# Kernel tuning notes

Measured on AMD Instinct MI355X. Metric: run time of the kernel, lower is better.

Reference implementation:

```python
import jax, jax.numpy as jnp
import numpy as np

H, W = 256, 256
N = H * W
C0, C1, C2 = 16, 32, 64  # base, base*2, base*4


def _grid_edges(h, w):
    """8-neighborhood grid edges (directed, both directions) + self loops."""
    idx = np.arange(h * w).reshape(h, w)
    srcs, dsts = [], []
    for dy in (-1, 0, 1):
        for dx in (-1, 0, 1):
            if dy == 0 and dx == 0:
                continue
            s = idx[max(0, -dy):h - max(0, dy), max(0, -dx):w - max(0, dx)]
            d = idx[max(0, dy):h - max(0, -dy), max(0, dx):w - max(0, -dx)]
            srcs.append(s.ravel()); dsts.append(d.ravel())
    srcs.append(np.arange(h * w)); dsts.append(np.arange(h * w))  # GATConv add_self_loops
    return np.concatenate(srcs).astype(np.int32), np.concatenate(dsts).astype(np.int32)


def _conv2d(x, w, b, pad):
    y = jax.lax.conv_general_dilated(x, w, (1, 1), [(pad, pad), (pad, pad)],
                                     dimension_numbers=('NCHW', 'OIHW', 'NCHW'))
    return y + b[None, :, None, None]


def _bn(x, g, b, eps=1e-5):
    # training-mode BatchNorm2d: biased batch statistics over (N,H,W)
    mu = x.mean((0, 2, 3), keepdims=True)
    var = ((x - mu) ** 2).mean((0, 2, 3), keepdims=True)
    return g[None, :, None, None] * (x - mu) * jax.lax.rsqrt(var + eps) + b[None, :, None, None]


def _gat(xg, w, a_s, a_d, b, src, dst):
    # PyG GATConv, heads=1: gather -> leaky_relu attention -> softmax over dst -> scatter-add
    def one(xn):
        h = xn @ w.T                                   # [N, C_out]
        e = jax.nn.leaky_relu((h @ a_s)[src] + (h @ a_d)[dst], 0.2)  # [E]
        m = jax.ops.segment_max(e, dst, num_segments=N)
        p = jnp.exp(e - m[dst])
        denom = jax.ops.segment_sum(p, dst, num_segments=N)
        agg = jax.ops.segment_sum(h[src] * p[:, None], dst, num_segments=N)
        return agg / (denom[:, None] + 1e-16) + b
    return jax.vmap(one)(xg)


def _gcb(x, pos_w, pos_b, gw, gas, gad, gb, src, dst):
    B, C = x.shape[0], x.shape[1]
    px = jnp.linspace(-1.0, 1.0, W)
    py = jnp.linspace(-1.0, 1.0, H)
    gx, gy = jnp.meshgrid(px, py, indexing='xy')       # each (H, W)
    pos = jnp.stack([gy, gx], -1)                      # (H, W, 2)
    pe = pos @ pos_w.T + pos_b                         # (H, W, C)
    x = x + pe.transpose(2, 0, 1)[None]
    xg = x.transpose(0, 2, 3, 1).reshape(B, N, C)      # batch of disjoint graphs -> vmap
    out = _gat(xg, gw, gas, gad, gb, src, dst)
    return out.reshape(B, H, W, -1).transpose(0, 3, 1, 2)


def _forward(x, conv1_w, conv1_b, bn1_g, bn1_b,
             pos1_w, pos1_b, gat1_w, gat1_as, gat1_ad, gat1_b, bn2_g, bn2_b,
             pos2_w, pos2_b, gat2_w, gat2_as, gat2_ad, gat2_b, bn3_g, bn3_b,
             mlp1_w, mlp1_b, mlp2_w, mlp2_b, filt, filt_bias,
             enh1_w, enh1_b, enh2_w, enh2_b, bn4_g, bn4_b, src, dst):
    f = _bn(jax.nn.relu(_conv2d(x, conv1_w, conv1_b, 2)), bn1_g, bn1_b)
    f = _bn(jax.nn.relu(_gcb(f, pos1_w, pos1_b, gat1_w, gat1_as, gat1_ad, gat1_b, src, dst)), bn2_g, bn2_b)
    f = _bn(jax.nn.relu(_gcb(f, pos2_w, pos2_b, gat2_w, gat2_as, gat2_ad, gat2_b, src, dst)), bn3_g, bn3_b)
    pooled = f.mean((2, 3))                            # AdaptiveAvgPool2d(1)
    h = jax.nn.relu(pooled @ mlp1_w.T + mlp1_b)
    cw = jax.nn.softmax(h @ mlp2_w.T + mlp2_b, axis=1)[:, :, None, None]
    wf = f * cw
    ff = wf * filt + filt_bias
    enh = _conv2d(jax.nn.relu(_conv2d(ff, enh1_w, enh1_b, 1)), enh2_w, enh2_b, 1) + ff
    return _bn(jax.nn.relu(enh), bn4_g, bn4_b)


def setup_inputs() -> dict:
    key = jax.random.key(0)
    ks = iter(jax.random.split(key, 40))
    def rn(shape, s=0.1):
        return jax.random.normal(next(ks), shape, dtype=jnp.float32) * s
    src, dst = _grid_edges(H, W)
    return {
        'x': jax.random.normal(next(ks), (2, 1, H, W), dtype=jnp.float32),
        'conv1_w': rn((C0, 1, 5, 5)), 'conv1_b': rn((C0,)),
        'bn1_g': jnp.ones((C0,)), 'bn1_b': jnp.zeros((C0,)),
        'pos1_w': rn((C0, 2)), 'pos1_b': rn((C0,)),
        'gat1_w': rn((C1, C0)), 'gat1_as': rn((C1,)), 'gat1_ad': rn((C1,)), 'gat1_b': rn((C1,)),
        'bn2_g': jnp.ones((C1,)), 'bn2_b': jnp.zeros((C1,)),
        'pos2_w': rn((C1, 2)), 'pos2_b': rn((C1,)),
        'gat2_w': rn((C2, C1)), 'gat2_as': rn((C2,)), 'gat2_ad': rn((C2,)), 'gat2_b': rn((C2,)),
        'bn3_g': jnp.ones((C2,)), 'bn3_b': jnp.zeros((C2,)),
        'mlp1_w': rn((C2 // 4, C2)), 'mlp1_b': rn((C2 // 4,)),
        'mlp2_w': rn((C2, C2 // 4)), 'mlp2_b': rn((C2,)),
        'filt': jnp.ones((1, C2, H, W)), 'filt_bias': jnp.zeros((1, C2, 1, 1)),
        'enh1_w': rn((C2 // 2, C2, 3, 3)), 'enh1_b': rn((C2 // 2,)),
        'enh2_w': rn((C2, C2 // 2, 3, 3)), 'enh2_b': rn((C2,)),
        'bn4_g': jnp.ones((C2,)), 'bn4_b': jnp.zeros((C2,)),
        'src': jnp.asarray(src), 'dst': jnp.asarray(dst),
    }


def reference(x, conv1_w, conv1_b, bn1_g, bn1_b,
              pos1_w, pos1_b, gat1_w, gat1_as, gat1_ad, gat1_b, bn2_g, bn2_b,
              pos2_w, pos2_b, gat2_w, gat2_as, gat2_ad, gat2_b, bn3_g, bn3_b,
              mlp1_w, mlp1_b, mlp2_w, mlp2_b, filt, filt_bias,
              enh1_w, enh1_b, enh2_w, enh2_b, bn4_g, bn4_b, src, dst):
    return _forward(x, conv1_w, conv1_b, bn1_g, bn1_b,
                    pos1_w, pos1_b, gat1_w, gat1_as, gat1_ad, gat1_b, bn2_g, bn2_b,
                    pos2_w, pos2_b, gat2_w, gat2_as, gat2_ad, gat2_b, bn3_g, bn3_b,
                    mlp1_w, mlp1_b, mlp2_w, mlp2_b, filt, filt_bias,
                    enh1_w, enh1_b, enh2_w, enh2_b, bn4_g, bn4_b, src, dst)
```

## Files before the change

kernel.cpp:

```cpp
#include <hip/hip_runtime.h>
#include <math.h>

#define HH 256
#define WW 256
#define NPIX 65536
#define BATCH 2

#define OFF_W0   0u
#define OFF_W1   8388608u
#define OFF_W2   16777216u
#define OFF_W3   20971520u
#define OFF_S    25165824u
#define OFF_D    25296896u
#define OFF_STAT 25427968u
#define OFF_ST1  (OFF_STAT + 0u)
#define OFF_ST2  (OFF_STAT + 64u)
#define OFF_ST3  (OFF_STAT + 192u)
#define OFF_ST4  (OFF_STAT + 448u)
#define OFF_CW   (OFF_STAT + 576u)
#define STAT_ZERO_N 704
#define OFF_WB1  (OFF_STAT + 704u)
#define OFF_WB2  (OFF_WB1 + 18432u)

typedef __attribute__((ext_vector_type(8))) short bf8v;
typedef __attribute__((ext_vector_type(4))) float f4v;
typedef __attribute__((ext_vector_type(4))) unsigned short us4;

#define GLL16(g, l) __builtin_amdgcn_global_load_lds(                               \
    (const __attribute__((address_space(1))) unsigned int*)(g),                    \
    (__attribute__((address_space(3))) unsigned int*)(l), 16, 0, 0)

__device__ __forceinline__ unsigned short f2bf(float f) {
    unsigned u = __float_as_uint(f);
    return (unsigned short)((u + 0x7FFFu + ((u >> 16) & 1u)) >> 16);
}
__device__ __forceinline__ float bf2f(unsigned short u) {
    return __uint_as_float(((unsigned)u) << 16);
}

__device__ __forceinline__ void bn_coef(const float* __restrict__ raw,
                                        const float* __restrict__ g,
                                        const float* __restrict__ b,
                                        int C, int c, float& A, float& Bv) {
    const float inv = 1.f / (float)(BATCH * NPIX);
    float mu  = raw[c] * inv;
    float var = raw[C + c] * inv - mu * mu;
    float rinv = rsqrtf(var + 1e-5f);
    A  = g[c] * rinv;
    Bv = b[c] - A * mu;
}

__device__ __forceinline__ void wave_red2(float& s, float& q) {
#pragma unroll
    for (int off = 32; off; off >>= 1) {
        s += __shfl_xor(s, off);
        q += __shfl_xor(q, off);
    }
}

__device__ __forceinline__ void row_swz512(int bid, int& y, int& b) {
    int orig = (bid & 7) * 64 + (bid >> 3);
    y = orig & 255;
    b = orig >> 8;
}

__global__ void prep(float* __restrict__ st,
                     const float* __restrict__ w1, unsigned short* __restrict__ wb1,
                     const float* __restrict__ w2, unsigned short* __restrict__ wb2) {
    int bid = blockIdx.x, tid = threadIdx.x;
    if (bid < 3) {
        int i = bid * 256 + tid;
        if (i < STAT_ZERO_N) st[i] = 0.f;
    } else if (bid < 75) {
        int i = (bid - 3) * 256 + tid;
        int co = i / (64 * 9);
        int rem = i - co * 64 * 9;
        int ci = rem / 9;
        int pos = rem - ci * 9;
        wb1[(pos * 32 + co) * 64 + ci] = f2bf(w1[i]);
    } else {
        int i = (bid - 75) * 256 + tid;
        int co = i / (32 * 9);
        int rem = i - co * 32 * 9;
        int ci = rem / 9;
        int pos = rem - ci * 9;
        wb2[(pos * 64 + co) * 32 + ci] = f2bf(w2[i]);
    }
}

__global__ __launch_bounds__(256) void conv5x5_all(const float* __restrict__ x,
                                                   const float* __restrict__ w,
                                                   const float* __restrict__ bias,
                                                   unsigned short* __restrict__ out,
                                                   float* __restrict__ st) {
    int y = blockIdx.x, b = blockIdx.y;
    int xx = threadIdx.x;
    __shared__ float lds[5 * 260];
    __shared__ float red[2][16][4];
    for (int i = threadIdx.x; i < 5 * 260; i += 256) {
        int r = i / 260, pos = i - r * 260;
        int yy = y + r - 2, xc = pos - 2;
        float v = 0.f;
        if ((unsigned)yy < 256u && (unsigned)xc < 256u) v = x[(b << 16) + (yy << 8) + xc];
        lds[i] = v;
    }
    __syncthreads();
    float v[25];
#pragma unroll
    for (int r = 0; r < 5; r++)
#pragma unroll
        for (int c = 0; c < 5; c++) v[r * 5 + c] = lds[r * 260 + xx + c];
    int lane = threadIdx.x & 63, wv = threadIdx.x >> 6;
#pragma unroll
    for (int co = 0; co < 16; co++) {
        float acc = bias[co];
#pragma unroll
        for (int k = 0; k < 25; k++) acc = fmaf(v[k], w[co * 25 + k], acc);
        acc = fmaxf(acc, 0.f);
        out[((size_t)(b * 16 + co) << 16) + (y << 8) + xx] = f2bf(acc);
        float s = acc, q = acc * acc;
        wave_red2(s, q);
        if (lane == 0) { red[0][co][wv] = s; red[1][co][wv] = q; }
    }
    __syncthreads();
    if (threadIdx.x < 16) {
        int co = threadIdx.x;
        float s = red[0][co][0] + red[0][co][1] + red[0][co][2] + red[0][co][3];
        float q = red[1][co][0] + red[1][co][1] + red[1][co][2] + red[1][co][3];
        atomicAdd(&st[co], s);
        atomicAdd(&st[16 + co], q);
    }
}

template <int CI, int CO>
__global__ void gat_pre(const unsigned short* __restrict__ f, const float* __restrict__ raw,
                        const float* __restrict__ bng, const float* __restrict__ bnb,
                        const float* __restrict__ posw, const float* __restrict__ posb,
                        const float* __restrict__ gw, const float* __restrict__ gas,
                        const float* __restrict__ gad,
                        unsigned short* __restrict__ hout, float* __restrict__ sout,
                        float* __restrict__ dout) {
    int tid = blockIdx.x * 256 + threadIdx.x;
    int n = tid & (NPIX - 1);
    int b = tid >> 16;
    int y = n >> 8, x = n & 255;
    float py = y * (2.f / 255.f) - 1.f;
    float px = x * (2.f / 255.f) - 1.f;
    float v[CI];
#pragma unroll
    for (int ci = 0; ci < CI; ci++) {
        float A, Bv;
        bn_coef(raw, bng, bnb, CI, ci, A, Bv);
        float t = fmaf(bf2f(f[(size_t)(b * CI + ci) * NPIX + n]), A, Bv);
        v[ci] = t + posw[2 * ci] * py + posw[2 * ci + 1] * px + posb[ci];
    }
    float s = 0.f, d = 0.f;
    for (int co = 0; co < CO; co++) {
        float acc = 0.f;
#pragma unroll
        for (int ci = 0; ci < CI; ci++) acc = fmaf(v[ci], gw[co * CI + ci], acc);
        hout[(size_t)(b * CO + co) * NPIX + n] = f2bf(acc);
        s = fmaf(acc, gas[co], s);
        d = fmaf(acc, gad[co], d);
    }
    sout[tid] = s;
    dout[tid] = d;
}

template <int CO, bool POOL>
__global__ __launch_bounds__(256) void gat_stencil_mfma(const unsigned short* __restrict__ hb,
                                                        const float* __restrict__ sbuf,
                                                        const float* __restrict__ dbuf,
                                                        const float* __restrict__ gb,
                                                        unsigned short* __restrict__ out,
                                                        float* __restrict__ st) {
    constexpr int NT = CO / 16;
    int y, b;
    row_swz512(blockIdx.x, y, b);
    int tid = threadIdx.x, lane = tid & 63, wid = tid >> 6;
    int m = lane & 15, grp = lane >> 4;
    int xw = wid * 64;
    {
        int x = xw + lane;
        float di = dbuf[(b << 16) + (y << 8) + x];
        float p[9], mx = -1e30f;
#pragma unroll
        for (int k = 0; k < 9; k++) {
            int dy = k / 3 - 1, dx = k % 3 - 1;
            int yy = y + dy, xx = x + dx;
            bool ok = ((unsigned)yy < 256u) && ((unsigned)xx < 256u);
            float e = -1e30f;
            if (ok) {
                float t = sbuf[(b << 16) + (yy << 8) + xx] + di;
                e = t > 0.f ? t : 0.2f * t;
            }
            p[k] = e;
            mx = fmaxf(mx, e);
        }
        float den = 0.f;
#pragma unroll
        for (int k = 0; k < 9; k++) { p[k] = __expf(p[k] - mx); den += p[k]; }
        float rden = 1.f / (den + 1e-16f);
        unsigned short pb[9];
#pragma unroll
        for (int k = 0; k < 9; k++) pb[k] = f2bf(p[k] * rden);
        unsigned pk0 = (unsigned)pb[0] | ((unsigned)pb[1] << 16);
        unsigned pk1 = (unsigned)pb[2] | ((unsigned)pb[3] << 16);
        unsigned pk2 = (unsigned)pb[4] | ((unsigned)pb[5] << 16);
        unsigned pk3 = (unsigned)pb[6] | ((unsigned)pb[7] << 16);
        unsigned pk4 = (unsigned)pb[8];
        float sAcc[NT], qAcc[NT], bb[NT];
#pragma unroll
        for (int ct = 0; ct < NT; ct++) { sAcc[ct] = 0.f; qAcc[ct] = 0.f; bb[ct] = gb[ct * 16 + m]; }

#pragma unroll 1
        for (int t = 0; t < 4; t++) {
            int xb = xw + t * 16;
            int src = t * 16 + m;
            unsigned rk0 = __shfl(pk0, src);
            unsigned rk1 = __shfl(pk1, src);
            unsigned rk2 = __shfl(pk2, src);
            unsigned rk3 = __shfl(pk3, src);
            unsigned rk4 = __shfl(pk4, src);
            unsigned short rb[9];
            rb[0] = (unsigned short)rk0; rb[1] = (unsigned short)(rk0 >> 16);
            rb[2] = (unsigned short)rk1; rb[3] = (unsigned short)(rk1 >> 16);
            rb[4] = (unsigned short)rk2; rb[5] = (unsigned short)(rk2 >> 16);
            rb[6] = (unsigned short)rk3; rb[7] = (unsigned short)(rk3 >> 16);
            rb[8] = (unsigned short)rk4;
            union { bf8v v; unsigned short h[8]; } af[3];
#pragma unroll
            for (int dyi = 0; dyi < 3; dyi++)
#pragma unroll
                for (int j = 0; j < 8; j++) {
                    int k = grp * 8 + j;
                    int d = k - 8 - m;
                    af[dyi].h[j] = (d >= -1 && d <= 1) ? rb[dyi * 3 + d + 1] : (unsigned short)0;
                }
            f4v acc[NT];
            f4v z4 = {0.f, 0.f, 0.f, 0.f};
#pragma unroll
            for (int ct = 0; ct < NT; ct++) acc[ct] = z4;
            int px0 = xb - 8 + grp * 8;
            px0 = px0 < 0 ? 0 : (px0 > 248 ? 248 : px0);
#pragma unroll
            for (int dyi = 0; dyi < 3; dyi++) {
                int yy = y + dyi - 1;
                if ((unsigned)yy >= 256u) continue;
#pragma unroll
                for (int ct = 0; ct < NT; ct++) {
                    bf8v bv = *(const bf8v*)(hb + (((size_t)(b * CO + ct * 16 + m)) << 16) + (yy << 8) + px0);
                    acc[ct] = __builtin_amdgcn_mfma_f32_16x16x32_bf16(af[dyi].v, bv, acc[ct], 0, 0, 0);
                }
            }
            int pxr = xb + grp * 4;
#pragma unroll
            for (int ct = 0; ct < NT; ct++) {
                f4v a = acc[ct];
                float o0 = fmaxf(a[0] + bb[ct], 0.f);
                float o1 = fmaxf(a[1] + bb[ct], 0.f);
                float o2 = fmaxf(a[2] + bb[ct], 0.f);
                float o3 = fmaxf(a[3] + bb[ct], 0.f);
                us4 pkst = {f2bf(o0), f2bf(o1), f2bf(o2), f2bf(o3)};
                *(us4*)(out + (((size_t)(b * CO + ct * 16 + m)) << 16) + (y << 8) + pxr) = pkst;
                sAcc[ct] += o0 + o1 + o2 + o3;
                qAcc[ct] += o0 * o0 + o1 * o1 + o2 * o2 + o3 * o3;
            }
        }
#pragma unroll
        for (int ct = 0; ct < NT; ct++) {
            sAcc[ct] += __shfl_xor(sAcc[ct], 16); sAcc[ct] += __shfl_xor(sAcc[ct], 32);
            qAcc[ct] += __shfl_xor(qAcc[ct], 16); qAcc[ct] += __shfl_xor(qAcc[ct], 32);
        }
        __shared__ float red[2][NT][16][4];
        if (grp == 0) {
#pragma unroll
            for (int ct = 0; ct < NT; ct++) {
                red[0][ct][m][wid] = sAcc[ct];
                red[1][ct][m][wid] = qAcc[ct];
            }
        }
        __syncthreads();
        if (tid < CO) {
            int ct = tid >> 4, mm = tid & 15;
            float s = red[0][ct][mm][0] + red[0][ct][mm][1] + red[0][ct][mm][2] + red[0][ct][mm][3];
            float qq = red[1][ct][mm][0] + red[1][ct][mm][1] + red[1][ct][mm][2] + red[1][ct][mm][3];
            atomicAdd(&st[tid], s);
            atomicAdd(&st[CO + tid], qq);
            if (POOL) atomicAdd(&st[2 * CO + b * CO + tid], s);
        }
    }
}

__global__ void mlp_cw(const float* __restrict__ raw3, const float* __restrict__ g3,
                       const float* __restrict__ b3, const float* __restrict__ w1,
                       const float* __restrict__ bb1, const float* __restrict__ w2,
                       const float* __restrict__ bb2, float* __restrict__ cw) {
    __shared__ float pooled[2][64];
    __shared__ float hsh[2][16];
    int tid = threadIdx.x;
    {
        int b = tid >> 6, c = tid & 63;
        float A, Bv;
        bn_coef(raw3, g3, b3, 64, c, A, Bv);
        float sm = raw3[128 + (b << 6) + c];
        pooled[b][c] = fmaf(sm * (1.f / 65536.f), A, Bv);
    }
    __syncthreads();
    if (tid < 32) {
        int b = tid >> 4, j = tid & 15;
        float acc = bb1[j];
        for (int c2 = 0; c2 < 64; c2++) acc = fmaf(pooled[b][c2], w1[(j << 6) + c2], acc);
        hsh[b][j] = fmaxf(acc, 0.f);
    }
    __syncthreads();
    int b = tid >> 6, c = tid & 63;
    float logit = bb2[c];
    for (int j = 0; j < 16; j++) logit = fmaf(hsh[b][j], w2[(c << 4) + j], logit);
    float mm = logit;
#pragma unroll
    for (int off = 32; off; off >>= 1) mm = fmaxf(mm, __shfl_xor(mm, off));
    float e = __expf(logit - mm);
    float ss = e;
#pragma unroll
    for (int off = 32; off; off >>= 1) ss += __shfl_xor(ss, off);
    cw[(b << 6) + c] = e / ss;
}

__global__ __launch_bounds__(256) void ff_t(const unsigned short* __restrict__ g64,
                                            const float* __restrict__ raw3,
                                            const float* __restrict__ g3,
                                            const float* __restrict__ b3,
                                            const float* __restrict__ cw,
                                            const float* __restrict__ filt,
                                            const float* __restrict__ fbias,
                                            float* __restrict__ ffout,
                                            unsigned* __restrict__ at1) {
    int pxb = blockIdx.x * 64;
    int b = pxb >> 16;
    int nb = pxb & 65535;
    __shared__ unsigned t[64 * 33];
    int tid = threadIdx.x;
#pragma unroll
    for (int k = 0; k < 2; k++) {
        int u = tid + k * 256;
        int q = u & 15;
        int cp = u >> 4;
        int ch0 = cp * 2, ch1 = ch0 + 1;
        float A0, B0, A1, B1;
        bn_coef(raw3, g3, b3, 64, ch0, A0, B0);
        bn_coef(raw3, g3, b3, 64, ch1, A1, B1);
        float s0 = cw[(b << 6) + ch0], s1 = cw[(b << 6) + ch1];
        float fb0 = fbias[ch0], fb1 = fbias[ch1];
        int n = nb + q * 4;
        us4 r0 = *(const us4*)(g64 + ((size_t)(b * 64 + ch0) << 16) + n);
        us4 r1 = *(const us4*)(g64 + ((size_t)(b * 64 + ch1) << 16) + n);
        float4 l0 = *(const float4*)(filt + ((size_t)ch0 << 16) + n);
        float4 l1 = *(const float4*)(filt + ((size_t)ch1 << 16) + n);
        float4 o0, o1;
        o0.x = fmaf(fmaf(bf2f(r0[0]), A0, B0) * s0, l0.x, fb0);
        o0.y = fmaf(fmaf(bf2f(r0[1]), A0, B0) * s0, l0.y, fb0);
        o0.z = fmaf(fmaf(bf2f(r0[2]), A0, B0) * s0, l0.z, fb0);
        o0.w = fmaf(fmaf(bf2f(r0[3]), A0, B0) * s0, l0.w, fb0);
        o1.x = fmaf(fmaf(bf2f(r1[0]), A1, B1) * s1, l1.x, fb1);
        o1.y = fmaf(fmaf(bf2f(r1[1]), A1, B1) * s1, l1.y, fb1);
        o1.z = fmaf(fmaf(bf2f(r1[2]), A1, B1) * s1, l1.z, fb1);
        o1.w = fmaf(fmaf(bf2f(r1[3]), A1, B1) * s1, l1.w, fb1);
        *(float4*)(ffout + ((size_t)(b * 64 + ch0) << 16) + n) = o0;
        *(float4*)(ffout + ((size_t)(b * 64 + ch1) << 16) + n) = o1;
        float e0[4] = {o0.x, o0.y, o0.z, o0.w};
        float e1[4] = {o1.x, o1.y, o1.z, o1.w};
#pragma unroll
        for (int i = 0; i < 4; i++)
            t[(q * 4 + i) * 33 + cp] = (unsigned)f2bf(e0[i]) | ((unsigned)f2bf(e1[i]) << 16);
    }
    __syncthreads();
#pragma unroll
    for (int j = 0; j < 8; j++) {
        int lin = j * 256 + tid;
        int pl = lin >> 5, cp = lin & 31;
        unsigned v = t[pl * 33 + cp];
        int P = pxb + pl;
        size_t byte = ((size_t)P << 7) + ((cp >= 16) ? 64 : 0)
                    + (((cp & 15) * 4) ^ (((P >> 1) & 3) << 4));
        *(unsigned*)((char*)at1 + byte) = v;
    }
}

__global__ __launch_bounds__(256) void enh1_mfma(const unsigned short* __restrict__ at1,
                                                 const unsigned short* __restrict__ wb,
                                                 const float* __restrict__ bias,
                                                 unsigned short* __restrict__ at2) {
    int y, b;
    row_swz512(blockIdx.x, y, b);
    int tid = threadIdx.x;
    int lane = tid & 63, wid = tid >> 6;
    __shared__ __align__(16) unsigned short lds_u16[3 * 258 * 32];
    char* ldsb = (char*)lds_u16;
    {
        bf8v z = {0, 0, 0, 0, 0, 0, 0, 0};
        for (int i = tid; i < 3 * 258 * 32 / 8; i += 256) ((bf8v*)lds_u16)[i] = z;
    }
    f4v acc[4][2];
    {
        f4v z4 = {0.f, 0.f, 0.f, 0.f};
#pragma unroll
        for (int m = 0; m < 4; m++) { acc[m][0] = z4; acc[m][1] = z4; }
    }
#pragma unroll 1
    for (int kh = 0; kh < 2; kh++) {
        __syncthreads();
        for (int c = wid; c < 48; c += 4) {
            int r = c >> 4, k = c & 15;
            int yy = y + r - 1;
            if ((unsigned)yy < 256u) {
                const char* src = (const char*)at1
                    + (((size_t)((b << 16) + (yy << 8)) + (k * 16 + (lane >> 2))) << 7)
                    + kh * 64 + (lane & 3) * 16;
                char* dst = ldsb + (r * 258 + 1) * 64 + k * 1024;
                GLL16(src, dst);
            }
        }
        __syncthreads();
        bf8v bw0[9], bw1[9];
#pragma unroll
        for (int pos = 0; pos < 9; pos++) {
            bw0[pos] = *(const bf8v*)(wb + (pos * 32 + (lane & 15)) * 64 + kh * 32 + (lane >> 4) * 8);
            bw1[pos] = *(const bf8v*)(wb + (pos * 32 + 16 + (lane & 15)) * 64 + kh * 32 + (lane >> 4) * 8);
        }
#pragma unroll
        for (int mt = 0; mt < 4; mt++) {
            int xb = (wid * 4 + mt) * 16 + (lane & 15);
#pragma unroll
            for (int ky = 0; ky < 3; ky++) {
#pragma unroll
                for (int kx = 0; kx < 3; kx++) {
                    int x = xb + kx - 1;
                    int s = x + 1;
                    int off = (ky * 258 + s) * 64 + (((lane >> 4) * 16) ^ (((x >> 1) & 3) << 4));
                    bf8v a = *(const bf8v*)(ldsb + off);
                    acc[mt][0] = __builtin_amdgcn_mfma_f32_16x16x32_bf16(a, bw0[ky * 3 + kx], acc[mt][0], 0, 0, 0);
                    acc[mt][1] = __builtin_amdgcn_mfma_f32_16x16x32_bf16(a, bw1[ky * 3 + kx], acc[mt][1], 0, 0, 0);
                }
            }
        }
    }
    float bb[2] = {bias[lane & 15], bias[16 + (lane & 15)]};
#pragma unroll
    for (int mt = 0; mt < 4; mt++) {
#pragma unroll
        for (int nt = 0; nt < 2; nt++) {
            f4v v = acc[mt][nt];
            int co = nt * 16 + (lane & 15);
#pragma unroll
            for (int r = 0; r < 4; r++) {
                int x = (wid * 4 + mt) * 16 + (lane >> 4) * 4 + r;
                float val = fmaxf(v[r] + bb[nt], 0.f);
                size_t byte = (((size_t)((b << 16) + (y << 8) + x)) << 6)
                            + ((co * 2) ^ (((x >> 1) & 3) << 4));
                *(unsigned short*)((char*)at2 + byte) = f2bf(val);
            }
        }
    }
}

__global__ __launch_bounds__(256) void enh2_mfma(const unsigned short* __restrict__ at2,
                                                 const unsigned short* __restrict__ wb,
                                                 const float* __restrict__ bias,
                                                 const float* __restrict__ ff,
                                                 float* __restrict__ out,
                                                 float* __restrict__ st) {
    int y, b;
    row_swz512(blockIdx.x, y, b);
    int tid = threadIdx.x;
    int lane = tid & 63, wid = tid >> 6;
    __shared__ __align__(16) unsigned short lds_u16[3 * 258 * 32];
    char* ldsb = (char*)lds_u16;
    {
        bf8v z = {0, 0, 0, 0, 0, 0, 0, 0};
        for (int i = tid; i < 3 * 258 * 32 / 8; i += 256) ((bf8v*)lds_u16)[i] = z;
    }
    __syncthreads();
    for (int c = wid; c < 48; c += 4) {
        int r = c >> 4, k = c & 15;
        int yy = y + r - 1;
        if ((unsigned)yy < 256u) {
            const char* src = (const char*)at2
                + (((size_t)((b << 16) + (yy << 8))) << 6) + k * 1024 + lane * 16;
            char* dst = ldsb + (r * 258 + 1) * 64 + k * 1024;
            GLL16(src, dst);
        }
    }
    __syncthreads();
    f4v acc[4][4];
    {
        f4v z4 = {0.f, 0.f, 0.f, 0.f};
#pragma unroll
        for (int m = 0; m < 4; m++)
#pragma unroll
            for (int n = 0; n < 4; n++) acc[m][n] = z4;
    }
#pragma unroll
    for (int np = 0; np < 2; np++) {
        bf8v bw0[9], bw1[9];
#pragma unroll
        for (int pos = 0; pos < 9; pos++) {
            bw0[pos] = *(const bf8v*)(wb + (pos * 64 + np * 32 + (lane & 15)) * 32 + (lane >> 4) * 8);
            bw1[pos] = *(const bf8v*)(wb + (pos * 64 + np * 32 + 16 + (lane & 15)) * 32 + (lane >> 4) * 8);
        }
#pragma unroll
        for (int mt = 0; mt < 4; mt++) {
            int xb = (wid * 4 + mt) * 16 + (lane & 15);
#pragma unroll
            for (int ky = 0; ky < 3; ky++) {
#pragma unroll
                for (int kx = 0; kx < 3; kx++) {
                    int x = xb + kx - 1;
                    int s = x + 1;
                    int off = (ky * 258 + s) * 64 + (((lane >> 4) * 16) ^ (((x >> 1) & 3) << 4));
                    bf8v a = *(const bf8v*)(ldsb + off);
                    acc[mt][2 * np]     = __builtin_amdgcn_mfma_f32_16x16x32_bf16(a, bw0[ky * 3 + kx], acc[mt][2 * np], 0, 0, 0);
                    acc[mt][2 * np + 1] = __builtin_amdgcn_mfma_f32_16x16x32_bf16(a, bw1[ky * 3 + kx], acc[mt][2 * np + 1], 0, 0, 0);
                }
            }
        }
    }
    __syncthreads();
    float* red = (float*)lds_u16;
#pragma unroll
    for (int nt = 0; nt < 4; nt++) {
        int co = nt * 16 + (lane & 15);
        float bb = bias[co];
        float s = 0.f, q = 0.f;
#pragma unroll
        for (int mt = 0; mt < 4; mt++) {
            int xb4 = (wid * 4 + mt) * 16 + (lane >> 4) * 4;
            size_t idx = ((size_t)(b * 64 + co) << 16) + (y << 8) + xb4;
            float4 res = *(const float4*)(ff + idx);
            f4v a = acc[mt][nt];
            float4 o;
            o.x = fmaxf(a[0] + bb + res.x, 0.f);
            o.y = fmaxf(a[1] + bb + res.y, 0.f);
            o.z = fmaxf(a[2] + bb + res.z, 0.f);
            o.w = fmaxf(a[3] + bb + res.w, 0.f);
            *(float4*)(out + idx) = o;
            s += o.x + o.y + o.z + o.w;
            q += o.x * o.x + o.y * o.y + o.z * o.z + o.w * o.w;
        }
        s += __shfl_xor(s, 16); s += __shfl_xor(s, 32);
        q += __shfl_xor(q, 16); q += __shfl_xor(q, 32);
        if (lane < 16) {
            red[(co * 4 + wid) * 2 + 0] = s;
            red[(co * 4 + wid) * 2 + 1] = q;
        }
    }
    __syncthreads();
    if (tid < 64) {
        float s = 0.f, q = 0.f;
#pragma unroll
        for (int w = 0; w < 4; w++) {
            s += red[(tid * 4 + w) * 2 + 0];
            q += red[(tid * 4 + w) * 2 + 1];
        }
        atomicAdd(&st[tid], s);
        atomicAdd(&st[64 + tid], q);
    }
}

__global__ void bn_apply4(float4* __restrict__ io, const float* __restrict__ raw,
                          const float* __restrict__ g, const float* __restrict__ b) {
    int t = blockIdx.x * 256 + threadIdx.x;
    int c = (t >> 14) & 63;
    float A, Bv;
    bn_coef(raw, g, b, 64, c, A, Bv);
    float4 v = io[t];
    v.x = fmaf(v.x, A, Bv);
    v.y = fmaf(v.y, A, Bv);
    v.z = fmaf(v.z, A, Bv);
    v.w = fmaf(v.w, A, Bv);
    io[t] = v;
}

extern "C" void kernel_launch(void* const* d_in, const int* in_sizes, int n_in,
                              void* d_out, int out_size, void* d_ws, size_t ws_size,
                              hipStream_t stream) {
    const float* x       = (const float*)d_in[0];
    const float* conv1_w = (const float*)d_in[1];
    const float* conv1_b = (const float*)d_in[2];
    const float* bn1_g   = (const float*)d_in[3];
    const float* bn1_b   = (const float*)d_in[4];
    const float* pos1_w  = (const float*)d_in[5];
    const float* pos1_b  = (const float*)d_in[6];
    const float* gat1_w  = (const float*)d_in[7];
    const float* gat1_as = (const float*)d_in[8];
    const float* gat1_ad = (const float*)d_in[9];
    const float* gat1_b  = (const float*)d_in[10];
    const float* bn2_g   = (const float*)d_in[11];
    const float* bn2_b   = (const float*)d_in[12];
    const float* pos2_w  = (const float*)d_in[13];
    const float* pos2_b  = (const float*)d_in[14];
    const float* gat2_w  = (const float*)d_in[15];
    const float* gat2_as = (const float*)d_in[16];
    const float* gat2_ad = (const float*)d_in[17];
    const float* gat2_b  = (const float*)d_in[18];
    const float* bn3_g   = (const float*)d_in[19];
    const float* bn3_b   = (const float*)d_in[20];
    const float* mlp1_w  = (const float*)d_in[21];
    const float* mlp1_b  = (const float*)d_in[22];
    const float* mlp2_w  = (const float*)d_in[23];
    const float* mlp2_b  = (const float*)d_in[24];
    const float* filt    = (const float*)d_in[25];
    const float* fbias   = (const float*)d_in[26];
    const float* enh1_w  = (const float*)d_in[27];
    const float* enh1_b  = (const float*)d_in[28];
    const float* enh2_w  = (const float*)d_in[29];
    const float* enh2_b  = (const float*)d_in[30];
    const float* bn4_g   = (const float*)d_in[31];
    const float* bn4_b   = (const float*)d_in[32];

    float* ws = (float*)d_ws;
    unsigned short* P0 = (unsigned short*)(ws + OFF_W0);
    unsigned short* HB = (unsigned short*)(ws + OFF_W1);
    float* FF = ws + OFF_W1;
    unsigned* AT1 = (unsigned*)(ws + OFF_W2);
    unsigned short* AT2 = (unsigned short*)(ws + OFF_W3);
    float* SB = ws + OFF_S;
    float* DB = ws + OFF_D;
    float* ST1 = ws + OFF_ST1;
    float* ST2 = ws + OFF_ST2;
    float* ST3 = ws + OFF_ST3;
    float* ST4 = ws + OFF_ST4;
    float* CW  = ws + OFF_CW;
    unsigned short* WB1 = (unsigned short*)(ws + OFF_WB1);
    unsigned short* WB2 = (unsigned short*)(ws + OFF_WB2);
    float* out = (float*)d_out;

    prep<<<147, 256, 0, stream>>>(ws + OFF_STAT, enh1_w, WB1, enh2_w, WB2);

    conv5x5_all<<<dim3(256, 2), 256, 0, stream>>>(x, conv1_w, conv1_b, P0, ST1);

    gat_pre<16, 32><<<512, 256, 0, stream>>>(P0, ST1, bn1_g, bn1_b, pos1_w, pos1_b,
                                             gat1_w, gat1_as, gat1_ad, HB, SB, DB);

    gat_stencil_mfma<32, false><<<512, 256, 0, stream>>>(HB, SB, DB, gat1_b, P0, ST2);

    gat_pre<32, 64><<<512, 256, 0, stream>>>(P0, ST2, bn2_g, bn2_b, pos2_w, pos2_b,
                                             gat2_w, gat2_as, gat2_ad, HB, SB, DB);

    gat_stencil_mfma<64, true><<<512, 256, 0, stream>>>(HB, SB, DB, gat2_b, P0, ST3);

    mlp_cw<<<1, 128, 0, stream>>>(ST3, bn3_g, bn3_b, mlp1_w, mlp1_b, mlp2_w, mlp2_b, CW);

    ff_t<<<2048, 256, 0, stream>>>(P0, ST3, bn3_g, bn3_b, CW, filt, fbias, FF, AT1);

    enh1_mfma<<<512, 256, 0, stream>>>((const unsigned short*)AT1, WB1, enh1_b, AT2);

    enh2_mfma<<<512, 256, 0, stream>>>(AT2, WB2, enh2_b, FF, out, ST4);

    bn_apply4<<<32768 / 4, 256, 0, stream>>>((float4*)out, ST4, bn4_g, bn4_b);
}
```

Before: 197.0 us.

## Split GAT stencil blocks by channel half and store FF residual as bf16

```diff
diff --git a/kernel.cpp b/kernel.cpp
--- a/kernel.cpp
+++ b/kernel.cpp
@@ -174,121 +174,129 @@
                                                         const float* __restrict__ gb,
                                                         unsigned short* __restrict__ out,
                                                         float* __restrict__ st) {
-    constexpr int NT = CO / 16;
-    int y, b;
-    row_swz512(blockIdx.x, y, b);
+    constexpr int NT2 = CO / 32;
+    constexpr int CH = CO / 2;
+    int bid = blockIdx.x;
+    int orig = (bid & 7) * 128 + (bid >> 3);
+    int coh = orig & 1;
+    int rowu = orig >> 1;
+    int y = rowu & 255;
+    int b = rowu >> 8;
     int tid = threadIdx.x, lane = tid & 63, wid = tid >> 6;
     int m = lane & 15, grp = lane >> 4;
     int xw = wid * 64;
-    {
-        int x = xw + lane;
-        float di = dbuf[(b << 16) + (y << 8) + x];
-        float p[9], mx = -1e30f;
-#pragma unroll
-        for (int k = 0; k < 9; k++) {
-            int dy = k / 3 - 1, dx = k % 3 - 1;
-            int yy = y + dy, xx = x + dx;
-            bool ok = ((unsigned)yy < 256u) && ((unsigned)xx < 256u);
-            float e = -1e30f;
-            if (ok) {
-                float t = sbuf[(b << 16) + (yy << 8) + xx] + di;
-                e = t > 0.f ? t : 0.2f * t;
+    int x = xw + lane;
+    float di = dbuf[(b << 16) + (y << 8) + x];
+    float p[9], mx = -1e30f;
+#pragma unroll
+    for (int k = 0; k < 9; k++) {
+        int dy = k / 3 - 1, dx = k % 3 - 1;
+        int yy = y + dy, xxn = x + dx;
+        bool ok = ((unsigned)yy < 256u) && ((unsigned)xxn < 256u);
+        float e = -1e30f;
+        if (ok) {
+            float t = sbuf[(b << 16) + (yy << 8) + xxn] + di;
+            e = t > 0.f ? t : 0.2f * t;
+        }
+        p[k] = e;
+        mx = fmaxf(mx, e);
+    }
+    float den = 0.f;
+#pragma unroll
+    for (int k = 0; k < 9; k++) { p[k] = __expf(p[k] - mx); den += p[k]; }
+    float rden = 1.f / (den + 1e-16f);
+    unsigned short pb[9];
+#pragma unroll
+    for (int k = 0; k < 9; k++) pb[k] = f2bf(p[k] * rden);
+    unsigned pk0 = (unsigned)pb[0] | ((unsigned)pb[1] << 16);
+    unsigned pk1 = (unsigned)pb[2] | ((unsigned)pb[3] << 16);
+    unsigned pk2 = (unsigned)pb[4] | ((unsigned)pb[5] << 16);
+    unsigned pk3 = (unsigned)pb[6] | ((unsigned)pb[7] << 16);
+    unsigned pk4 = (unsigned)pb[8];
+    float sAcc[NT2], qAcc[NT2], bb[NT2];
+#pragma unroll
+    for (int ct = 0; ct < NT2; ct++) {
+        sAcc[ct] = 0.f; qAcc[ct] = 0.f;
+        bb[ct] = gb[coh * CH + ct * 16 + m];
+    }
+#pragma unroll 1
+    for (int t = 0; t < 4; t++) {
+        int xb = xw + t * 16;
+        int src = t * 16 + m;
+        unsigned rk0 = __shfl(pk0, src);
+        unsigned rk1 = __shfl(pk1, src);
+        unsigned rk2 = __shfl(pk2, src);
+        unsigned rk3 = __shfl(pk3, src);
+        unsigned rk4 = __shfl(pk4, src);
+        unsigned short rb[9];
+        rb[0] = (unsigned short)rk0; rb[1] = (unsigned short)(rk0 >> 16);
+        rb[2] = (unsigned short)rk1; rb[3] = (unsigned short)(rk1 >> 16);
+        rb[4] = (unsigned short)rk2; rb[5] = (unsigned short)(rk2 >> 16);
+        rb[6] = (unsigned short)rk3; rb[7] = (unsigned short)(rk3 >> 16);
+        rb[8] = (unsigned short)rk4;
+        union { bf8v v; unsigned short h[8]; } af[3];
+#pragma unroll
+        for (int dyi = 0; dyi < 3; dyi++)
+#pragma unroll
+            for (int j = 0; j < 8; j++) {
+                int k = grp * 8 + j;
+                int d = k - 8 - m;
+                af[dyi].h[j] = (d >= -1 && d <= 1) ? rb[dyi * 3 + d + 1] : (unsigned short)0;
             }
-            p[k] = e;
-            mx = fmaxf(mx, e);
-        }
-        float den = 0.f;
-#pragma unroll
-        for (int k = 0; k < 9; k++) { p[k] = __expf(p[k] - mx); den += p[k]; }
-        float rden = 1.f / (den + 1e-16f);
-        unsigned short pb[9];
-#pragma unroll
-        for (int k = 0; k < 9; k++) pb[k] = f2bf(p[k] * rden);
-        unsigned pk0 = (unsigned)pb[0] | ((unsigned)pb[1] << 16);
-        unsigned pk1 = (unsigned)pb[2] | ((unsigned)pb[3] << 16);
-        unsigned pk2 = (unsigned)pb[4] | ((unsigned)pb[5] << 16);
-        unsigned pk3 = (unsigned)pb[6] | ((unsigned)pb[7] << 16);
-        unsigned pk4 = (unsigned)pb[8];
-        float sAcc[NT], qAcc[NT], bb[NT];
-#pragma unroll
-        for (int ct = 0; ct < NT; ct++) { sAcc[ct] = 0.f; qAcc[ct] = 0.f; bb[ct] = gb[ct * 16 + m]; }
-
-#pragma unroll 1
-        for (int t = 0; t < 4; t++) {
-            int xb = xw + t * 16;
-            int src = t * 16 + m;
-            unsigned rk0 = __shfl(pk0, src);
-            unsigned rk1 = __shfl(pk1, src);
-            unsigned rk2 = __shfl(pk2, src);
-            unsigned rk3 = __shfl(pk3, src);
-            unsigned rk4 = __shfl(pk4, src);
-            unsigned short rb[9];
-            rb[0] = (unsigned short)rk0; rb[1] = (unsigned short)(rk0 >> 16);
-            rb[2] = (unsigned short)rk1; rb[3] = (unsigned short)(rk1 >> 16);
-            rb[4] = (unsigned short)rk2; rb[5] = (unsigned short)(rk2 >> 16);
-            rb[6] = (unsigned short)rk3; rb[7] = (unsigned short)(rk3 >> 16);
-            rb[8] = (unsigned short)rk4;
-            union { bf8v v; unsigned short h[8]; } af[3];
-#pragma unroll
-            for (int dyi = 0; dyi < 3; dyi++)
-#pragma unroll
-                for (int j = 0; j < 8; j++) {
-                    int k = grp * 8 + j;
-                    int d = k - 8 - m;
-                    af[dyi].h[j] = (d >= -1 && d <= 1) ? rb[dyi * 3 + d + 1] : (unsigned short)0;
-                }
-            f4v acc[NT];
-            f4v z4 = {0.f, 0.f, 0.f, 0.f};
-#pragma unroll
-            for (int ct = 0; ct < NT; ct++) acc[ct] = z4;
-            int px0 = xb - 8 + grp * 8;
-            px0 = px0 < 0 ? 0 : (px0 > 248 ? 248 : px0);
-#pragma unroll
-            for (int dyi = 0; dyi < 3; dyi++) {
-                int yy = y + dyi - 1;
-                if ((unsigned)yy >= 256u) continue;
-#pragma unroll
-                for (int ct = 0; ct < NT; ct++) {
-                    bf8v bv = *(const bf8v*)(hb + (((size_t)(b * CO + ct * 16 + m)) << 16) + (yy << 8) + px0);
-                    acc[ct] = __builtin_amdgcn_mfma_f32_16x16x32_bf16(af[dyi].v, bv, acc[ct], 0, 0, 0);
-                }
+        f4v acc[NT2];
+        f4v z4 = {0.f, 0.f, 0.f, 0.f};
+#pragma unroll
+        for (int ct = 0; ct < NT2; ct++) acc[ct] = z4;
+        int px0 = xb - 8 + grp * 8;
+        px0 = px0 < 0 ? 0 : (px0 > 248 ? 248 : px0);
+#pragma unroll
+        for (int dyi = 0; dyi < 3; dyi++) {
+            int yy = y + dyi - 1;
+            if ((unsigned)yy >= 256u) continue;
+#pragma unroll
+            for (int ct = 0; ct < NT2; ct++) {
+                int ch = coh * CH + ct * 16 + m;
+                bf8v bv = *(const bf8v*)(hb + (((size_t)(b * CO + ch)) << 16) + (yy << 8) + px0);
+                acc[ct] = __builtin_amdgcn_mfma_f32_16x16x32_bf16(af[dyi].v, bv, acc[ct], 0, 0, 0);
             }
-            int pxr = xb + grp * 4;
-#pragma unroll
-            for (int ct = 0; ct < NT; ct++) {
-                f4v a = acc[ct];
-                float o0 = fmaxf(a[0] + bb[ct], 0.f);
-                float o1 = fmaxf(a[1] + bb[ct], 0.f);
-                float o2 = fmaxf(a[2] + bb[ct], 0.f);
-                float o3 = fmaxf(a[3] + bb[ct], 0.f);
-                us4 pkst = {f2bf(o0), f2bf(o1), f2bf(o2), f2bf(o3)};
-                *(us4*)(out + (((size_t)(b * CO + ct * 16 + m)) << 16) + (y << 8) + pxr) = pkst;
-                sAcc[ct] += o0 + o1 + o2 + o3;
-                qAcc[ct] += o0 * o0 + o1 * o1 + o2 * o2 + o3 * o3;
-            }
-        }
-#pragma unroll
-        for (int ct = 0; ct < NT; ct++) {
-            sAcc[ct] += __shfl_xor(sAcc[ct], 16); sAcc[ct] += __shfl_xor(sAcc[ct], 32);
-            qAcc[ct] += __shfl_xor(qAcc[ct], 16); qAcc[ct] += __shfl_xor(qAcc[ct], 32);
-        }
-        __shared__ float red[2][NT][16][4];
-        if (grp == 0) {
-#pragma unroll
-            for (int ct = 0; ct < NT; ct++) {
-                red[0][ct][m][wid] = sAcc[ct];
-                red[1][ct][m][wid] = qAcc[ct];
-            }
-        }
-        __syncthreads();
-        if (tid < CO) {
-            int ct = tid >> 4, mm = tid & 15;
-            float s = red[0][ct][mm][0] + red[0][ct][mm][1] + red[0][ct][mm][2] + red[0][ct][mm][3];
-            float qq = red[1][ct][mm][0] + red[1][ct][mm][1] + red[1][ct][mm][2] + red[1][ct][mm][3];
-            atomicAdd(&st[tid], s);
-            atomicAdd(&st[CO + tid], qq);
-            if (POOL) atomicAdd(&st[2 * CO + b * CO + tid], s);
-        }
+        }
+        int pxr = xb + grp * 4;
+#pragma unroll
+        for (int ct = 0; ct < NT2; ct++) {
+            int ch = coh * CH + ct * 16 + m;
+            f4v a = acc[ct];
+            float o0 = fmaxf(a[0] + bb[ct], 0.f);
+            float o1 = fmaxf(a[1] + bb[ct], 0.f);
+            float o2 = fmaxf(a[2] + bb[ct], 0.f);
+            float o3 = fmaxf(a[3] + bb[ct], 0.f);
+            us4 pkst = {f2bf(o0), f2bf(o1), f2bf(o2), f2bf(o3)};
+            *(us4*)(out + (((size_t)(b * CO + ch)) << 16) + (y << 8) + pxr) = pkst;
+            sAcc[ct] += o0 + o1 + o2 + o3;
+            qAcc[ct] += o0 * o0 + o1 * o1 + o2 * o2 + o3 * o3;
+        }
+    }
+#pragma unroll
+    for (int ct = 0; ct < NT2; ct++) {
+        sAcc[ct] += __shfl_xor(sAcc[ct], 16); sAcc[ct] += __shfl_xor(sAcc[ct], 32);
+        qAcc[ct] += __shfl_xor(qAcc[ct], 16); qAcc[ct] += __shfl_xor(qAcc[ct], 32);
+    }
+    __shared__ float red[2][NT2][16][4];
+    if (grp == 0) {
+#pragma unroll
+        for (int ct = 0; ct < NT2; ct++) {
+            red[0][ct][m][wid] = sAcc[ct];
+            red[1][ct][m][wid] = qAcc[ct];
+        }
+    }
+    __syncthreads();
+    if (tid < CH) {
+        int ct = tid >> 4, mm = tid & 15;
+        int c = coh * CH + tid;
+        float s = red[0][ct][mm][0] + red[0][ct][mm][1] + red[0][ct][mm][2] + red[0][ct][mm][3];
+        float qq = red[1][ct][mm][0] + red[1][ct][mm][1] + red[1][ct][mm][2] + red[1][ct][mm][3];
+        atomicAdd(&st[c], s);
+        atomicAdd(&st[CO + c], qq);
+        if (POOL) atomicAdd(&st[2 * CO + b * CO + c], s);
     }
 }
 
@@ -334,7 +342,7 @@
                                             const float* __restrict__ cw,
                                             const float* __restrict__ filt,
                                             const float* __restrict__ fbias,
-                                            float* __restrict__ ffout,
+                                            unsigned short* __restrict__ ffout,
                                             unsigned* __restrict__ at1) {
     int pxb = blockIdx.x * 64;
     int b = pxb >> 16;
@@ -366,13 +374,13 @@
         o1.y = fmaf(fmaf(bf2f(r1[1]), A1, B1) * s1, l1.y, fb1);
         o1.z = fmaf(fmaf(bf2f(r1[2]), A1, B1) * s1, l1.z, fb1);
         o1.w = fmaf(fmaf(bf2f(r1[3]), A1, B1) * s1, l1.w, fb1);
-        *(float4*)(ffout + ((size_t)(b * 64 + ch0) << 16) + n) = o0;
-        *(float4*)(ffout + ((size_t)(b * 64 + ch1) << 16) + n) = o1;
-        float e0[4] = {o0.x, o0.y, o0.z, o0.w};
-        float e1[4] = {o1.x, o1.y, o1.z, o1.w};
+        us4 f0 = {f2bf(o0.x), f2bf(o0.y), f2bf(o0.z), f2bf(o0.w)};
+        us4 f1 = {f2bf(o1.x), f2bf(o1.y), f2bf(o1.z), f2bf(o1.w)};
+        *(us4*)(ffout + ((size_t)(b * 64 + ch0) << 16) + n) = f0;
+        *(us4*)(ffout + ((size_t)(b * 64 + ch1) << 16) + n) = f1;
 #pragma unroll
         for (int i = 0; i < 4; i++)
-            t[(q * 4 + i) * 33 + cp] = (unsigned)f2bf(e0[i]) | ((unsigned)f2bf(e1[i]) << 16);
+            t[(q * 4 + i) * 33 + cp] = (unsigned)f0[i] | ((unsigned)f1[i] << 16);
     }
     __syncthreads();
 #pragma unroll
@@ -467,7 +475,7 @@
 __global__ __launch_bounds__(256) void enh2_mfma(const unsigned short* __restrict__ at2,
                                                  const unsigned short* __restrict__ wb,
                                                  const float* __restrict__ bias,
-                                                 const float* __restrict__ ff,
+                                                 const unsigned short* __restrict__ ff,
                                                  float* __restrict__ out,
                                                  float* __restrict__ st) {
     int y, b;
@@ -536,13 +544,13 @@
         for (int mt = 0; mt < 4; mt++) {
             int xb4 = (wid * 4 + mt) * 16 + (lane >> 4) * 4;
             size_t idx = ((size_t)(b * 64 + co) << 16) + (y << 8) + xb4;
-            float4 res = *(const float4*)(ff + idx);
+            us4 rv = *(const us4*)(ff + idx);
             f4v a = acc[mt][nt];
             float4 o;
-            o.x = fmaxf(a[0] + bb + res.x, 0.f);
-            o.y = fmaxf(a[1] + bb + res.y, 0.f);
-            o.z = fmaxf(a[2] + bb + res.z, 0.f);
-            o.w = fmaxf(a[3] + bb + res.w, 0.f);
+            o.x = fmaxf(a[0] + bb + bf2f(rv[0]), 0.f);
+            o.y = fmaxf(a[1] + bb + bf2f(rv[1]), 0.f);
+            o.z = fmaxf(a[2] + bb + bf2f(rv[2]), 0.f);
+            o.w = fmaxf(a[3] + bb + bf2f(rv[3]), 0.f);
             *(float4*)(out + idx) = o;
             s += o.x + o.y + o.z + o.w;
             q += o.x * o.x + o.y * o.y + o.z * o.z + o.w * o.w;
@@ -621,7 +629,7 @@
     float* ws = (float*)d_ws;
     unsigned short* P0 = (unsigned short*)(ws + OFF_W0);
     unsigned short* HB = (unsigned short*)(ws + OFF_W1);
-    float* FF = ws + OFF_W1;
+    unsigned short* FFB = (unsigned short*)(ws + OFF_W1);
     unsigned* AT1 = (unsigned*)(ws + OFF_W2);
     unsigned short* AT2 = (unsigned short*)(ws + OFF_W3);
     float* SB = ws + OFF_S;
@@ -642,20 +650,20 @@
     gat_pre<16, 32><<<512, 256, 0, stream>>>(P0, ST1, bn1_g, bn1_b, pos1_w, pos1_b,
                                              gat1_w, gat1_as, gat1_ad, HB, SB, DB);
 
-    gat_stencil_mfma<32, false><<<512, 256, 0, stream>>>(HB, SB, DB, gat1_b, P0, ST2);
+    gat_stencil_mfma<32, false><<<1024, 256, 0, stream>>>(HB, SB, DB, gat1_b, P0, ST2);
 
     gat_pre<32, 64><<<512, 256, 0, stream>>>(P0, ST2, bn2_g, bn2_b, pos2_w, pos2_b,
                                              gat2_w, gat2_as, gat2_ad, HB, SB, DB);
 
-    gat_stencil_mfma<64, true><<<512, 256, 0, stream>>>(HB, SB, DB, gat2_b, P0, ST3);
+    gat_stencil_mfma<64, true><<<1024, 256, 0, stream>>>(HB, SB, DB, gat2_b, P0, ST3);
 
     mlp_cw<<<1, 128, 0, stream>>>(ST3, bn3_g, bn3_b, mlp1_w, mlp1_b, mlp2_w, mlp2_b, CW);
 
-    ff_t<<<2048, 256, 0, stream>>>(P0, ST3, bn3_g, bn3_b, CW, filt, fbias, FF, AT1);
+    ff_t<<<2048, 256, 0, stream>>>(P0, ST3, bn3_g, bn3_b, CW, filt, fbias, FFB, AT1);
 
     enh1_mfma<<<512, 256, 0, stream>>>((const unsigned short*)AT1, WB1, enh1_b, AT2);
 
-    enh2_mfma<<<512, 256, 0, stream>>>(AT2, WB2, enh2_b, FF, out, ST4);
+    enh2_mfma<<<512, 256, 0, stream>>>(AT2, WB2, enh2_b, FFB, out, ST4);
 
     bn_apply4<<<32768 / 4, 256, 0, stream>>>((float4*)out, ST4, bn4_g, bn4_b);
 }
```

Result: faster. 189.4 us (-3.9%).
